# Kernel tuning notes

Measured on AMD Instinct MI355X. Metric: run time of the kernel, lower is better.

Reference implementation:

```python
import jax, jax.numpy as jnp
import numpy as np

N_STMT, N_FUNC = 100000, 50000
T, V, C, H, L, E = 16, 50000, 128, 8, 2, 200000
D = C // H  # per-head dim = 16
N_NODES = (N_STMT, N_FUNC)
# (src_type, dst_type) for the 3 relations: stmt->stmt, stmt->func, func->stmt
EDGE_TYPES = ((0, 0), (0, 1), (1, 0))


def _segment_softmax(logits, seg, num_segments):
    # logits: [E, H], seg: [E] destination node ids
    m = jax.ops.segment_max(logits, seg, num_segments)
    m = jnp.where(jnp.isfinite(m), m, 0.0)
    e = jnp.exp(logits - m[seg])
    s = jax.ops.segment_sum(e, seg, num_segments)
    return e / (s[seg] + 1e-16)


def setup_inputs() -> dict:
    key = jax.random.key(0)
    ks = jax.random.split(key, 24)
    nrm = lambda k, sh, s=0.1: jax.random.normal(k, sh, dtype=jnp.float32) * s
    ri = lambda k, sh, hi: jax.random.randint(k, sh, 0, hi, dtype=jnp.int32)
    return {
        "tok_stmt": ri(ks[0], (N_STMT, T), V),
        "tok_func": ri(ks[1], (N_FUNC, T), V),
        "e0_src": ri(ks[2], (E,), N_STMT), "e0_dst": ri(ks[3], (E,), N_STMT),
        "e1_src": ri(ks[4], (E,), N_STMT), "e1_dst": ri(ks[5], (E,), N_FUNC),
        "e2_src": ri(ks[6], (E,), N_FUNC), "e2_dst": ri(ks[7], (E,), N_STMT),
        "emb": nrm(ks[8], (V, C), 0.5),
        "lin_w": nrm(ks[9], (2, C, C)), "lin_b": jnp.zeros((2, C), jnp.float32),
        "kw": nrm(ks[10], (L, 2, C, C)), "kb": jnp.zeros((L, 2, C), jnp.float32),
        "qw": nrm(ks[11], (L, 2, C, C)), "qb": jnp.zeros((L, 2, C), jnp.float32),
        "vw": nrm(ks[12], (L, 2, C, C)), "vb": jnp.zeros((L, 2, C), jnp.float32),
        "aw": nrm(ks[13], (L, 2, C, C)), "ab": jnp.zeros((L, 2, C), jnp.float32),
        "skip": jnp.ones((L, 2), jnp.float32),
        "a_rel": nrm(ks[14], (L, 3, H, D, D), 0.25),
        "m_rel": nrm(ks[15], (L, 3, H, D, D), 0.25),
        "p_rel": jnp.ones((L, 3, H), jnp.float32),
    }


def _hgt_forward(tok_stmt, tok_func, edges, emb, lin_w, lin_b,
                 kw, kb, qw, qb, vw, vb, aw, ab, skip, a_rel, m_rel, p_rel):
    # STEncoder (embedding + mean pool) + relu, then per-type linear + relu
    xs = []
    for t, tok in enumerate((tok_stmt, tok_func)):
        e = jax.nn.relu(jnp.mean(emb[tok], axis=1))          # [N_t, C]
        xs.append(jax.nn.relu(e @ lin_w[t] + lin_b[t]))      # [N_t, C]

    scale = 1.0 / jnp.sqrt(jnp.float32(D))
    for l in range(L):
        k = [(x @ kw[l, t] + kb[l, t]).reshape(-1, H, D) for t, x in enumerate(xs)]
        q = [(x @ qw[l, t] + qb[l, t]).reshape(-1, H, D) for t, x in enumerate(xs)]
        v = [(x @ vw[l, t] + vb[l, t]).reshape(-1, H, D) for t, x in enumerate(xs)]
        agg = [jnp.zeros((N_NODES[t], H, D), xs[t].dtype) for t in range(2)]
        for r, (st, dt) in enumerate(EDGE_TYPES):
            src, dst = edges[r]
            k_r = jnp.einsum('nhd,hde->nhe', k[st], a_rel[l, r])
            v_r = jnp.einsum('nhd,hde->nhe', v[st], m_rel[l, r])
            logits = jnp.sum(q[dt][dst] * k_r[src], axis=-1) * p_rel[l, r] * scale  # [E,H]
            alpha = _segment_softmax(logits, dst, N_NODES[dt])
            msg = v_r[src] * alpha[..., None]                 # [E,H,D]
            agg[dt] = agg[dt] + jax.ops.segment_sum(msg, dst, N_NODES[dt])
        new_xs = []
        for t in range(2):
            o = jax.nn.gelu(agg[t].reshape(N_NODES[t], C))
            o = o @ aw[l, t] + ab[l, t]
            g = jax.nn.sigmoid(skip[l, t])
            new_xs.append(g * o + (1.0 - g) * xs[t])
        xs = new_xs
    return jnp.concatenate(xs, axis=0)  # [N_STMT + N_FUNC, C]


def reference(tok_stmt, tok_func, e0_src, e0_dst, e1_src, e1_dst, e2_src, e2_dst,
              emb, lin_w, lin_b, kw, kb, qw, qb, vw, vb, aw, ab, skip,
              a_rel, m_rel, p_rel):
    edges = ((e0_src, e0_dst), (e1_src, e1_dst), (e2_src, e2_dst))
    return _hgt_forward(tok_stmt, tok_func, edges, emb, lin_w, lin_b,
                        kw, kb, qw, qb, vw, vb, aw, ab, skip, a_rel, m_rel, p_rel)
```

## Files before the change

kernel.cpp:

```cpp
#include <hip/hip_runtime.h>
#include <hip/hip_bf16.h>


typedef __hip_bfloat16 bf16;
typedef __attribute__((ext_vector_type(8))) short short8;
typedef __attribute__((ext_vector_type(4))) short s4v;
typedef __attribute__((ext_vector_type(4))) float floatx4;

#define N_STMT 100000
#define N_FUNC 50000
#define N_TOT  150000
#define EDGES  200000
#define CCH 128
#define RPB 208
#define RPB2 96
#define GS2 1042
#define GF2 521

__device__ __forceinline__ float b2f(bf16 x){ return __bfloat162float(x); }
__device__ __forceinline__ float bs2f(short s){
  union { short s; bf16 h; } u; u.s = s; return __bfloat162float(u.h);
}
__device__ __forceinline__ short f2bs(float x){
  union { bf16 h; short s; } u; u.h = __float2bfloat16(x); return u.s;
}
__device__ __forceinline__ float blo(unsigned u){ return __uint_as_float(u << 16); }
__device__ __forceinline__ float bhi(unsigned u){ return __uint_as_float(u & 0xffff0000u); }
__device__ __forceinline__ float gelu_f(float x){
  float z = 1.5957691216057308f * (x + 0.044715f * x * x * x);
  float t = __expf(z);
  return x - x / (t + 1.f);
}

__global__ __launch_bounds__(256) void emb2bf(
    const float* __restrict__ emb, bf16* __restrict__ ebf)
{
  long i = ((long)blockIdx.x * 256 + threadIdx.x) * 8;
  float4 f0 = *(const float4*)(emb + i);
  float4 f1 = *(const float4*)(emb + i + 4);
  short8 o;
  o[0]=f2bs(f0.x); o[1]=f2bs(f0.y); o[2]=f2bs(f0.z); o[3]=f2bs(f0.w);
  o[4]=f2bs(f1.x); o[5]=f2bs(f1.y); o[6]=f2bs(f1.z); o[7]=f2bs(f1.w);
  *(short8*)(ebf + i) = o;
}

__global__ __launch_bounds__(256) void pool_embed(
    const int* __restrict__ tok_s, const int* __restrict__ tok_f,
    const bf16* __restrict__ ebf, bf16* __restrict__ E_out)
{
  int n = blockIdx.x * 4 + (threadIdx.x >> 6);
  int lane = threadIdx.x & 63, g = lane >> 4, c16 = lane & 15;
  const int* tok = (n < N_STMT) ? (tok_s + n * 16) : (tok_f + (n - N_STMT) * 16);
  float acc[8] = {0.f,0.f,0.f,0.f,0.f,0.f,0.f,0.f};
#pragma unroll
  for (int j = 0; j < 4; j++) {
    int v = tok[g * 4 + j];
    short8 row = *(const short8*)(ebf + (long)v * CCH + c16 * 8);
#pragma unroll
    for (int q = 0; q < 8; q++) acc[q] += bs2f(row[q]);
  }
#pragma unroll
  for (int q = 0; q < 8; q++) {
    acc[q] += __shfl_xor(acc[q], 16);
    acc[q] += __shfl_xor(acc[q], 32);
  }
  if (g == 0) {
    short8 o;
#pragma unroll
    for (int q = 0; q < 8; q++) o[q] = f2bs(fmaxf(acc[q] * (1.f/16.f), 0.f));
    *(short8*)(E_out + (long)n * CCH + c16 * 8) = o;
  }
}

__global__ __launch_bounds__(256) void transp_w(
    const float* __restrict__ lin_w, const float* __restrict__ qw,
    const float* __restrict__ aw, bf16* __restrict__ out)
{
  int mat = blockIdx.y;
  const float* src = (mat < 2) ? lin_w + mat * 16384
                   : (mat < 6) ? qw + (mat - 2) * 16384
                               : aw + (mat - 6) * 16384;
  bf16* dst = out + mat * 16384;
  int idx = blockIdx.x * 256 + threadIdx.x;
  int n = idx >> 7, k = idx & 127;
  dst[idx] = __float2bfloat16(src[k * 128 + n]);
}

__global__ __launch_bounds__(256) void make_wr_all(
    const float* __restrict__ kw, const float* __restrict__ kb,
    const float* __restrict__ vw, const float* __restrict__ vb,
    const float* __restrict__ a_rel, const float* __restrict__ m_rel,
    bf16* __restrict__ WRT, float* __restrict__ Bf)
{
  int y = blockIdx.y;
  bool isV = y >= 6;
  int z = isV ? y - 6 : y;
  int l = z / 3, r = z % 3, st = (r == 2) ? 1 : 0;
  const float* W   = (isV ? vw : kw) + (l * 2 + st) * 16384;
  const float* b   = (isV ? vb : kb) + (l * 2 + st) * 128;
  const float* rel = (isV ? m_rel : a_rel) + z * 2048;
  bf16* Wrt = WRT + y * 16384;
  float* br = Bf + y * 128;

  int idx = blockIdx.x * 256 + threadIdx.x;
  if (idx < 128 * 128) {
    int c = idx >> 7, o = idx & 127;
    int h = o >> 4, e = o & 15;
    float acc = 0.f;
#pragma unroll
    for (int d = 0; d < 16; d++)
      acc += W[c * 128 + h * 16 + d] * rel[h * 256 + d * 16 + e];
    Wrt[o * 128 + c] = __float2bfloat16(acc);
  }
  if (idx < 128) {
    int h = idx >> 4, e = idx & 15;
    float acc = 0.f;
#pragma unroll
    for (int d = 0; d < 16; d++)
      acc += b[h * 16 + d] * rel[h * 256 + d * 16 + e];
    br[idx] = acc;
  }
}

template <bool RELU, bool BLEND, bool OUT_BF16>
__global__ __launch_bounds__(256) void gemm_2t_reg(
    const bf16* __restrict__ Ab, const bf16* __restrict__ Wt0,
    const bf16* __restrict__ Wt1, const float* __restrict__ bias0,
    const float* __restrict__ bias1, const bf16* __restrict__ oldx,
    void* __restrict__ dstv, const float* __restrict__ skip2)
{
  const int wave = threadIdx.x >> 6, lane = threadIdx.x & 63;
  const int lane15 = lane & 15, quad = lane >> 4;
  const int jc0 = wave * 2;
  const int bid = blockIdx.x;
  const int type = (bid >= GS2);
  const long base = type ? (long)N_STMT * CCH : 0;
  const int Nrows = type ? N_FUNC : N_STMT;
  long row = (long)(type ? bid - GS2 : bid) * RPB2;
  long rowEnd = row + RPB2; if (rowEnd > Nrows) rowEnd = Nrows;
  const bf16* Wt = type ? Wt1 : Wt0;
  const float* bias = type ? bias1 : bias0;

  short8 w[2][4];
#pragma unroll
  for (int jj = 0; jj < 2; jj++)
#pragma unroll
    for (int kq = 0; kq < 4; kq++)
      w[jj][kq] = *(const short8*)(
          Wt + ((jc0 + jj) * 16 + lane15) * CCH + kq * 32 + quad * 8);
  float4 bb[2];
#pragma unroll
  for (int jj = 0; jj < 2; jj++)
    bb[jj] = *(const float4*)(bias + (jc0 + jj) * 16 + quad * 4);

  float g = 1.f, gi = 0.f;
  if (BLEND) {
    float sk = skip2[type];
    g = 1.f / (1.f + expf(-sk));
    gi = 1.f - g;
  }

  short8 a[4];
  {
    long r = row + lane15; if (r >= Nrows) r = Nrows - 1;
#pragma unroll
    for (int kq = 0; kq < 4; kq++)
      a[kq] = *(const short8*)(Ab + base + r * CCH + kq * 32 + quad * 8);
  }

  for (; row < rowEnd; row += 16) {
    short8 an[4];
    {
      long nrow = (row + 16 < rowEnd) ? row + 16 : row;
      long r = nrow + lane15; if (r >= Nrows) r = Nrows - 1;
#pragma unroll
      for (int kq = 0; kq < 4; kq++)
        an[kq] = *(const short8*)(Ab + base + r * CCH + kq * 32 + quad * 8);
    }

    floatx4 acc[2];
#pragma unroll
    for (int jj = 0; jj < 2; jj++) {
      acc[jj][0] = bb[jj].x; acc[jj][1] = bb[jj].y;
      acc[jj][2] = bb[jj].z; acc[jj][3] = bb[jj].w;
    }
#pragma unroll
    for (int kq = 0; kq < 4; kq++)
#pragma unroll
      for (int jj = 0; jj < 2; jj++)
        acc[jj] = __builtin_amdgcn_mfma_f32_16x16x32_bf16(
            w[jj][kq], a[kq], acc[jj], 0, 0, 0);

    long r = row + lane15;
    if (r < Nrows) {
#pragma unroll
      for (int jj = 0; jj < 2; jj++) {
        int c0 = (jc0 + jj) * 16 + quad * 4;
        long idx = base + r * CCH + c0;
        float v[4];
#pragma unroll
        for (int q = 0; q < 4; q++) v[q] = acc[jj][q];
        if (RELU) {
#pragma unroll
          for (int q = 0; q < 4; q++) v[q] = fmaxf(v[q], 0.f);
        }
        if (BLEND) {
          s4v ov = *(const s4v*)(oldx + idx);
#pragma unroll
          for (int q = 0; q < 4; q++) v[q] = g * v[q] + gi * bs2f(ov[q]);
        }
        if (OUT_BF16) {
          s4v o;
#pragma unroll
          for (int q = 0; q < 4; q++) o[q] = f2bs(v[q]);
          *(s4v*)((bf16*)dstv + idx) = o;
        } else {
          float4 o = make_float4(v[0], v[1], v[2], v[3]);
          *(float4*)((float*)dstv + idx) = o;
        }
      }
    }
#pragma unroll
    for (int kq = 0; kq < 4; kq++) a[kq] = an[kq];
  }
}

template <int NM>
__global__ __launch_bounds__(256, 2) void gemm_qkv_reg(
    const bf16* __restrict__ Ab,
    const bf16* __restrict__ W0, const float* __restrict__ B0,
    const bf16* __restrict__ W1, const float* __restrict__ B1,
    const bf16* __restrict__ W2, const float* __restrict__ B2,
    const bf16* __restrict__ W3, const float* __restrict__ B3,
    const bf16* __restrict__ W4, const float* __restrict__ B4,
    bf16* __restrict__ Q, bf16* __restrict__ KV0, bf16* __restrict__ KV1,
    int N)
{
  const int wave = threadIdx.x >> 6, lane = threadIdx.x & 63;
  const int lane15 = lane & 15, quad = lane >> 4;
  const int jc0 = wave * 2;

  long row = (long)blockIdx.x * RPB;
  if (row >= N) return;
  long rowEnd = row + RPB; if (rowEnd > N) rowEnd = N;

  const bf16* Wm[5]  = {W0, W1, W2, W3, W4};
  const float* Bm[5] = {B0, B1, B2, B3, B4};

  short8 w[NM][2][4];
#pragma unroll
  for (int m = 0; m < NM; m++)
#pragma unroll
    for (int jj = 0; jj < 2; jj++)
#pragma unroll
      for (int kq = 0; kq < 4; kq++)
        w[m][jj][kq] = *(const short8*)(
            Wm[m] + ((jc0 + jj) * 16 + lane15) * CCH + kq * 32 + quad * 8);

  short8 a[4];
  {
    long r = row + lane15; if (r >= N) r = N - 1;
#pragma unroll
    for (int kq = 0; kq < 4; kq++)
      a[kq] = *(const short8*)(Ab + r * CCH + kq * 32 + quad * 8);
  }

  for (; row < rowEnd; row += 16) {
    short8 an[4];
    {
      long nrow = (row + 16 < rowEnd) ? row + 16 : row;
      long r = nrow + lane15; if (r >= N) r = N - 1;
#pragma unroll
      for (int kq = 0; kq < 4; kq++)
        an[kq] = *(const short8*)(Ab + r * CCH + kq * 32 + quad * 8);
    }

    floatx4 acc[NM][2];
#pragma unroll
    for (int m = 0; m < NM; m++)
#pragma unroll
      for (int jj = 0; jj < 2; jj++) {
        float4 bb = *(const float4*)(Bm[m] + (jc0 + jj) * 16 + quad * 4);
        acc[m][jj][0] = bb.x; acc[m][jj][1] = bb.y;
        acc[m][jj][2] = bb.z; acc[m][jj][3] = bb.w;
      }

#pragma unroll
    for (int kq = 0; kq < 4; kq++)
#pragma unroll
      for (int m = 0; m < NM; m++)
#pragma unroll
        for (int jj = 0; jj < 2; jj++)
          acc[m][jj] = __builtin_amdgcn_mfma_f32_16x16x32_bf16(
              w[m][jj][kq], a[kq], acc[m][jj], 0, 0, 0);

    long r = row + lane15;
    if (r < N) {
#pragma unroll
      for (int jj = 0; jj < 2; jj++) {
        int c0 = (jc0 + jj) * 16 + quad * 4;
        s4v qo;
        qo[0] = f2bs(acc[0][jj][0]);
        qo[1] = f2bs(acc[0][jj][1]);
        qo[2] = f2bs(acc[0][jj][2]);
        qo[3] = f2bs(acc[0][jj][3]);
        *(s4v*)(Q + r * CCH + c0) = qo;

        short8 kv;
        kv[0] = f2bs(acc[1][jj][0]);
        kv[1] = f2bs(acc[1][jj][1]);
        kv[2] = f2bs(acc[2][jj][0]);
        kv[3] = f2bs(acc[2][jj][1]);
        kv[4] = f2bs(acc[1][jj][2]);
        kv[5] = f2bs(acc[1][jj][3]);
        kv[6] = f2bs(acc[2][jj][2]);
        kv[7] = f2bs(acc[2][jj][3]);
        *(short8*)(KV0 + r * 256 + 2 * c0) = kv;

        if constexpr (NM == 5) {
          kv[0] = f2bs(acc[3][jj][0]);
          kv[1] = f2bs(acc[3][jj][1]);
          kv[2] = f2bs(acc[4][jj][0]);
          kv[3] = f2bs(acc[4][jj][1]);
          kv[4] = f2bs(acc[3][jj][2]);
          kv[5] = f2bs(acc[3][jj][3]);
          kv[6] = f2bs(acc[4][jj][2]);
          kv[7] = f2bs(acc[4][jj][3]);
          *(short8*)(KV1 + r * 256 + 2 * c0) = kv;
        }
      }
    }
#pragma unroll
    for (int kq = 0; kq < 4; kq++) a[kq] = an[kq];
  }
}

__global__ __launch_bounds__(256) void csr_count(
    const int* __restrict__ dst, int* __restrict__ deg, int* __restrict__ pos)
{
  int e = blockIdx.x * 256 + threadIdx.x;
  if (e < EDGES) pos[e] = atomicAdd(&deg[dst[e]], 1);
}
__global__ __launch_bounds__(256) void csr_alloc(
    const int* __restrict__ deg, int* __restrict__ rowstart,
    int* __restrict__ total, int Ndst)
{
  int n = blockIdx.x * 256 + threadIdx.x;
  if (n < Ndst) rowstart[n] = atomicAdd(total, deg[n]);
}
__global__ __launch_bounds__(256) void csr_fill(
    const int* __restrict__ dst, const int* __restrict__ src,
    const int* __restrict__ rowstart, const int* __restrict__ pos,
    int* __restrict__ srcs)
{
  int e = blockIdx.x * 256 + threadIdx.x;
  if (e < EDGES) srcs[rowstart[dst[e]] + pos[e]] = src[e];
}

__device__ __forceinline__ void relmsg_grp(
    int rs, int g, const int* __restrict__ srcs,
    const bf16* __restrict__ KV, float psc,
    const float* __restrict__ q, int lane, float* __restrict__ out)
{
  int p = lane & 15;
  int gbase = lane & 48;
  float den = 0.f;
  float a[8] = {0.f,0.f,0.f,0.f,0.f,0.f,0.f,0.f};
  for (int j0 = 0; j0 < g; j0 += 16) {
    int rem = g - j0; if (rem > 16) rem = 16;
    int sl = srcs[rs + j0 + (p < rem ? p : rem - 1)];
    for (int j = 0; j < rem; j++) {
      int s = __shfl(sl, gbase + j);
      const bf16* rowp = KV + (long)s * 256 + 16 * p;
      uint4 u0 = *(const uint4*)(rowp);
      uint4 u1 = *(const uint4*)(rowp + 8);
      float prod = q[0]*blo(u0.x) + q[1]*bhi(u0.x)
                 + q[2]*blo(u0.z) + q[3]*bhi(u0.z)
                 + q[4]*blo(u1.x) + q[5]*bhi(u1.x)
                 + q[6]*blo(u1.z) + q[7]*bhi(u1.z);
      prod += __shfl_xor(prod, 1);
      float ev = __expf(prod * psc);
      den += ev;
      a[0] += ev * blo(u0.y); a[1] += ev * bhi(u0.y);
      a[2] += ev * blo(u0.w); a[3] += ev * bhi(u0.w);
      a[4] += ev * blo(u1.y); a[5] += ev * bhi(u1.y);
      a[6] += ev * blo(u1.w); a[7] += ev * bhi(u1.w);
    }
  }
  float inv = 1.f / (den + 1e-16f);
#pragma unroll
  for (int i = 0; i < 8; i++) out[i] = a[i] * inv;
}

__global__ __launch_bounds__(256) void agg_all(
    const int* __restrict__ rs0, const int* __restrict__ dg0, const int* __restrict__ srcs0,
    const int* __restrict__ rs1, const int* __restrict__ dg1, const int* __restrict__ srcs1,
    const int* __restrict__ rs2, const int* __restrict__ dg2, const int* __restrict__ srcs2,
    const bf16* __restrict__ KV0, const bf16* __restrict__ KV1,
    const bf16* __restrict__ KV2, const float* __restrict__ pl,
    const bf16* __restrict__ Qb, bf16* __restrict__ AGGb)
{
  int n = blockIdx.x * 16 + (threadIdx.x >> 4);
  if (n >= N_TOT) return;
  int lane = threadIdx.x & 63;
  int p = lane & 15, h = p >> 1;
  uint4 qv = *(const uint4*)(Qb + (long)n * CCH + 8 * p);
  float q[8];
  q[0] = blo(qv.x); q[1] = bhi(qv.x); q[2] = blo(qv.y); q[3] = bhi(qv.y);
  q[4] = blo(qv.z); q[5] = bhi(qv.z); q[6] = blo(qv.w); q[7] = bhi(qv.w);
  float m[8];
  if (n < N_STMT) {
    float m0[8], m2[8];
    relmsg_grp(rs0[n], dg0[n], srcs0, KV0, pl[h] * 0.25f, q, lane, m0);
    relmsg_grp(rs2[n], dg2[n], srcs2, KV2, pl[16 + h] * 0.25f, q, lane, m2);
#pragma unroll
    for (int i = 0; i < 8; i++) m[i] = m0[i] + m2[i];
  } else {
    int nf = n - N_STMT;
    relmsg_grp(rs1[nf], dg1[nf], srcs1, KV1, pl[8 + h] * 0.25f, q, lane, m);
  }
  short8 o;
#pragma unroll
  for (int i = 0; i < 8; i++) o[i] = f2bs(gelu_f(m[i]));
  *(short8*)(AGGb + (long)n * CCH + 8 * p) = o;
}

__global__ __launch_bounds__(256) void zero_out_k(float* __restrict__ out)
{
  long i = ((long)blockIdx.x * 256 + threadIdx.x) * 4;
  *(float4*)(out + i) = make_float4(0.f, 0.f, 0.f, 0.f);
}

extern "C" void kernel_launch(void* const* d_in, const int* in_sizes, int n_in,
                              void* d_out, int out_size, void* d_ws, size_t ws_size,
                              hipStream_t stream)
{
  const int* tok_s = (const int*)d_in[0];
  const int* tok_f = (const int*)d_in[1];
  const int* esrc[3] = {(const int*)d_in[2], (const int*)d_in[4], (const int*)d_in[6]};
  const int* edst[3] = {(const int*)d_in[3], (const int*)d_in[5], (const int*)d_in[7]};
  const float* emb   = (const float*)d_in[8];
  const float* lin_w = (const float*)d_in[9];
  const float* lin_b = (const float*)d_in[10];
  const float* kw = (const float*)d_in[11];
  const float* kb = (const float*)d_in[12];
  const float* qw = (const float*)d_in[13];
  const float* qb = (const float*)d_in[14];
  const float* vw = (const float*)d_in[15];
  const float* vb = (const float*)d_in[16];
  const float* aw = (const float*)d_in[17];
  const float* ab = (const float*)d_in[18];
  const float* skip  = (const float*)d_in[19];
  const float* a_rel = (const float*)d_in[20];
  const float* m_rel = (const float*)d_in[21];
  const float* p_rel = (const float*)d_in[22];

  float* Bf   = (float*)d_ws;
  bf16*  Xb   = (bf16*)(Bf + 1536);
  bf16*  AGGb = Xb  + 19200000L;
  bf16*  KV0  = AGGb + 19200000L;
  bf16*  KV1  = KV0 + 25600000L;
  bf16*  KV2  = KV1 + 25600000L;
  bf16*  WT   = KV2 + 12800000L;
  bf16*  WRT  = WT  + 163840L;
  int*   ip   = (int*)(WRT + 196608L);
  int* deg[3]      = {ip, ip + 100000, ip + 150000};
  int* total       = ip + 250000;
  int* rowstart[3] = {ip + 250004, ip + 350004, ip + 400004};
  int* srcs[3]     = {ip + 500004, ip + 700004, ip + 900004};
  int* pos         = ip + 1100004;
  bf16* EBF   = KV0;
  bf16*  Qb   = (bf16*)d_out;
  float* OUTF = (float*)d_out;

  const size_t NEED = (size_t)1536 * 4 + (size_t)102760448 * 2
                    + (size_t)1300004 * 4;
  if (ws_size < NEED) {
    zero_out_k<<<19200000 / 4 / 256, 256, 0, stream>>>(OUTF);
    return;
  }

  const int  Ntype[2] = {N_STMT, N_FUNC};
  const int  edt[3] = {0, 1, 0};
  const int  EB = (EDGES + 255) / 256;

  hipMemsetAsync(ip, 0, (size_t)250004 * 4, stream);
  for (int r = 0; r < 3; r++) {
    int Nd = Ntype[edt[r]];
    csr_count<<<EB, 256, 0, stream>>>(edst[r], deg[r], pos);
    csr_alloc<<<(Nd + 255) / 256, 256, 0, stream>>>(deg[r], rowstart[r], total + r, Nd);
    csr_fill<<<EB, 256, 0, stream>>>(edst[r], esrc[r], rowstart[r], pos, srcs[r]);
  }

  emb2bf<<<3125, 256, 0, stream>>>(emb, EBF);
  transp_w<<<dim3(64, 10), 256, 0, stream>>>(lin_w, qw, aw, WT);
  make_wr_all<<<dim3(64, 12), 256, 0, stream>>>(kw, kb, vw, vb, a_rel, m_rel, WRT, Bf);

  pool_embed<<<N_TOT / 4, 256, 0, stream>>>(tok_s, tok_f, EBF, AGGb);
  gemm_2t_reg<true, false, true><<<GS2 + GF2, 256, 0, stream>>>(
      AGGb, WT, WT + 16384, lin_b, lin_b + 128, nullptr, Xb, nullptr);

  const int GQS = (N_STMT + RPB - 1) / RPB;
  const int GQF = (N_FUNC + RPB - 1) / RPB;

  for (int l = 0; l < 2; l++) {
    int z0 = l * 3 + 0, z1 = l * 3 + 1, z2 = l * 3 + 2;
    gemm_qkv_reg<5><<<GQS, 256, 0, stream>>>(
        Xb,
        WT + (2 + l * 2) * 16384, qb + (l * 2) * 128,
        WRT + z0 * 16384, Bf + z0 * 128,
        WRT + (6 + z0) * 16384, Bf + (6 + z0) * 128,
        WRT + z1 * 16384, Bf + z1 * 128,
        WRT + (6 + z1) * 16384, Bf + (6 + z1) * 128,
        Qb, KV0, KV1, N_STMT);
    gemm_qkv_reg<3><<<GQF, 256, 0, stream>>>(
        Xb + (long)N_STMT * CCH,
        WT + (2 + l * 2 + 1) * 16384, qb + (l * 2 + 1) * 128,
        WRT + z2 * 16384, Bf + z2 * 128,
        WRT + (6 + z2) * 16384, Bf + (6 + z2) * 128,
        nullptr, nullptr, nullptr, nullptr,
        Qb + (long)N_STMT * CCH, KV2, nullptr, N_FUNC);
    agg_all<<<(N_TOT + 15) / 16, 256, 0, stream>>>(
        rowstart[0], deg[0], srcs[0], rowstart[1], deg[1], srcs[1],
        rowstart[2], deg[2], srcs[2], KV0, KV1, KV2,
        p_rel + l * 24, Qb, AGGb);
    if (l == 0)
      gemm_2t_reg<false, true, true><<<GS2 + GF2, 256, 0, stream>>>(
          AGGb, WT + 6 * 16384, WT + 7 * 16384, ab, ab + 128,
          Xb, Xb, skip);
    else
      gemm_2t_reg<false, true, false><<<GS2 + GF2, 256, 0, stream>>>(
          AGGb, WT + 8 * 16384, WT + 9 * 16384, ab + 256, ab + 384,
          Xb, OUTF, skip + 2);
  }
}
```

Baseline: 730.2 us.

## Split stmt QKV GEMM into two lighter kernels to raise occupancy

Splits the 5-matrix statement-node projection kernel into a Q+K+V kernel and a separate K+V kernel for the second relation. Each kernel now holds fewer weight registers, so launch bounds can allow 3–4 blocks per CU instead of 2. The change also drops the software prefetch of the next A tile and makes rows per block a runtime parameter (128 or 96). The trade-off is that the statement activations are read twice and there is one extra kernel launch per layer.

```diff
diff --git a/kernel.cpp b/kernel.cpp
--- a/kernel.cpp
+++ b/kernel.cpp
@@ -12,7 +12,6 @@
 #define N_TOT  150000
 #define EDGES  200000
 #define CCH 128
-#define RPB 208
 #define RPB2 96
 #define GS2 1042
 #define GF2 521
@@ -225,27 +224,26 @@
   }
 }
 
-template <int NM>
-__global__ __launch_bounds__(256, 2) void gemm_qkv_reg(
+template <int NM, bool HASQ>
+__global__ __launch_bounds__(256, (NM == 2 ? 4 : 3)) void gemm_qkv_reg(
     const bf16* __restrict__ Ab,
     const bf16* __restrict__ W0, const float* __restrict__ B0,
     const bf16* __restrict__ W1, const float* __restrict__ B1,
     const bf16* __restrict__ W2, const float* __restrict__ B2,
-    const bf16* __restrict__ W3, const float* __restrict__ B3,
-    const bf16* __restrict__ W4, const float* __restrict__ B4,
-    bf16* __restrict__ Q, bf16* __restrict__ KV0, bf16* __restrict__ KV1,
-    int N)
+    bf16* __restrict__ Q, bf16* __restrict__ KV, int N, int rpb)
 {
   const int wave = threadIdx.x >> 6, lane = threadIdx.x & 63;
   const int lane15 = lane & 15, quad = lane >> 4;
   const int jc0 = wave * 2;
-
-  long row = (long)blockIdx.x * RPB;
+  constexpr int KIDX = HASQ ? 1 : 0;
+  constexpr int VIDX = KIDX + 1;
+
+  long row = (long)blockIdx.x * rpb;
   if (row >= N) return;
-  long rowEnd = row + RPB; if (rowEnd > N) rowEnd = N;
-
-  const bf16* Wm[5]  = {W0, W1, W2, W3, W4};
-  const float* Bm[5] = {B0, B1, B2, B3, B4};
+  long rowEnd = row + rpb; if (rowEnd > N) rowEnd = N;
+
+  const bf16* Wm[3]  = {W0, W1, W2};
+  const float* Bm[3] = {B0, B1, B2};
 
   short8 w[NM][2][4];
 #pragma unroll
@@ -257,23 +255,13 @@
         w[m][jj][kq] = *(const short8*)(
             Wm[m] + ((jc0 + jj) * 16 + lane15) * CCH + kq * 32 + quad * 8);
 
-  short8 a[4];
-  {
-    long r = row + lane15; if (r >= N) r = N - 1;
+  for (; row < rowEnd; row += 16) {
+    long r = row + lane15;
+    long rc = (r < N) ? r : (N - 1);
+    short8 a[4];
 #pragma unroll
     for (int kq = 0; kq < 4; kq++)
-      a[kq] = *(const short8*)(Ab + r * CCH + kq * 32 + quad * 8);
-  }
-
-  for (; row < rowEnd; row += 16) {
-    short8 an[4];
-    {
-      long nrow = (row + 16 < rowEnd) ? row + 16 : row;
-      long r = nrow + lane15; if (r >= N) r = N - 1;
-#pragma unroll
-      for (int kq = 0; kq < 4; kq++)
-        an[kq] = *(const short8*)(Ab + r * CCH + kq * 32 + quad * 8);
-    }
+      a[kq] = *(const short8*)(Ab + rc * CCH + kq * 32 + quad * 8);
 
     floatx4 acc[NM][2];
 #pragma unroll
@@ -294,44 +282,30 @@
           acc[m][jj] = __builtin_amdgcn_mfma_f32_16x16x32_bf16(
               w[m][jj][kq], a[kq], acc[m][jj], 0, 0, 0);
 
-    long r = row + lane15;
     if (r < N) {
 #pragma unroll
       for (int jj = 0; jj < 2; jj++) {
         int c0 = (jc0 + jj) * 16 + quad * 4;
-        s4v qo;
-        qo[0] = f2bs(acc[0][jj][0]);
-        qo[1] = f2bs(acc[0][jj][1]);
-        qo[2] = f2bs(acc[0][jj][2]);
-        qo[3] = f2bs(acc[0][jj][3]);
-        *(s4v*)(Q + r * CCH + c0) = qo;
-
+        if constexpr (HASQ) {
+          s4v qo;
+          qo[0] = f2bs(acc[0][jj][0]);
+          qo[1] = f2bs(acc[0][jj][1]);
+          qo[2] = f2bs(acc[0][jj][2]);
+          qo[3] = f2bs(acc[0][jj][3]);
+          *(s4v*)(Q + r * CCH + c0) = qo;
+        }
         short8 kv;
-        kv[0] = f2bs(acc[1][jj][0]);
-        kv[1] = f2bs(acc[1][jj][1]);
-        kv[2] = f2bs(acc[2][jj][0]);
-        kv[3] = f2bs(acc[2][jj][1]);
-        kv[4] = f2bs(acc[1][jj][2]);
-        kv[5] = f2bs(acc[1][jj][3]);
-        kv[6] = f2bs(acc[2][jj][2]);
-        kv[7] = f2bs(acc[2][jj][3]);
-        *(short8*)(KV0 + r * 256 + 2 * c0) = kv;
-
-        if constexpr (NM == 5) {
-          kv[0] = f2bs(acc[3][jj][0]);
-          kv[1] = f2bs(acc[3][jj][1]);
-          kv[2] = f2bs(acc[4][jj][0]);
-          kv[3] = f2bs(acc[4][jj][1]);
-          kv[4] = f2bs(acc[3][jj][2]);
-          kv[5] = f2bs(acc[3][jj][3]);
-          kv[6] = f2bs(acc[4][jj][2]);
-          kv[7] = f2bs(acc[4][jj][3]);
-          *(short8*)(KV1 + r * 256 + 2 * c0) = kv;
-        }
+        kv[0] = f2bs(acc[KIDX][jj][0]);
+        kv[1] = f2bs(acc[KIDX][jj][1]);
+        kv[2] = f2bs(acc[VIDX][jj][0]);
+        kv[3] = f2bs(acc[VIDX][jj][1]);
+        kv[4] = f2bs(acc[KIDX][jj][2]);
+        kv[5] = f2bs(acc[KIDX][jj][3]);
+        kv[6] = f2bs(acc[VIDX][jj][2]);
+        kv[7] = f2bs(acc[VIDX][jj][3]);
+        *(short8*)(KV + r * 256 + 2 * c0) = kv;
       }
     }
-#pragma unroll
-    for (int kq = 0; kq < 4; kq++) a[kq] = an[kq];
   }
 }
 
@@ -500,26 +474,30 @@
   gemm_2t_reg<true, false, true><<<GS2 + GF2, 256, 0, stream>>>(
       AGGb, WT, WT + 16384, lin_b, lin_b + 128, nullptr, Xb, nullptr);
 
-  const int GQS = (N_STMT + RPB - 1) / RPB;
-  const int GQF = (N_FUNC + RPB - 1) / RPB;
+  const int GA = (N_STMT + 127) / 128;
+  const int GB = (N_STMT + 95) / 96;
+  const int GF = (N_FUNC + 127) / 128;
 
   for (int l = 0; l < 2; l++) {
     int z0 = l * 3 + 0, z1 = l * 3 + 1, z2 = l * 3 + 2;
-    gemm_qkv_reg<5><<<GQS, 256, 0, stream>>>(
+    gemm_qkv_reg<3, true><<<GA, 256, 0, stream>>>(
         Xb,
         WT + (2 + l * 2) * 16384, qb + (l * 2) * 128,
         WRT + z0 * 16384, Bf + z0 * 128,
         WRT + (6 + z0) * 16384, Bf + (6 + z0) * 128,
+        Qb, KV0, N_STMT, 128);
+    gemm_qkv_reg<2, false><<<GB, 256, 0, stream>>>(
+        Xb,
         WRT + z1 * 16384, Bf + z1 * 128,
         WRT + (6 + z1) * 16384, Bf + (6 + z1) * 128,
-        Qb, KV0, KV1, N_STMT);
-    gemm_qkv_reg<3><<<GQF, 256, 0, stream>>>(
+        nullptr, nullptr,
+        nullptr, KV1, N_STMT, 96);
+    gemm_qkv_reg<3, true><<<GF, 256, 0, stream>>>(
         Xb + (long)N_STMT * CCH,
         WT + (2 + l * 2 + 1) * 16384, qb + (l * 2 + 1) * 128,
         WRT + z2 * 16384, Bf + z2 * 128,
         WRT + (6 + z2) * 16384, Bf + (6 + z2) * 128,
-        nullptr, nullptr, nullptr, nullptr,
-        Qb + (long)N_STMT * CCH, KV2, nullptr, N_FUNC);
+        Qb + (long)N_STMT * CCH, KV2, N_FUNC, 128);
     agg_all<<<(N_TOT + 15) / 16, 256, 0, stream>>>(
         rowstart[0], deg[0], srcs[0], rowstart[1], deg[1], srcs[1],
         rowstart[2], deg[2], srcs[2], KV0, KV1, KV2,
```

Result: no change. 719.5 us (-1.5%).
